# Performance work log

Hardware: AMD Instinct MI355X
Metric: run time of the kernel (lower is better)

Reference implementation:

```python
import jax, jax.numpy as jnp
import numpy as np

D_MODEL = 1024
NUM_HEADS = 16
BATCH = 2
SEQ = 2048


def setup_inputs() -> dict:
    key = jax.random.key(0)
    ks = jax.random.split(key, 5)
    scale = 1.0 / np.sqrt(D_MODEL)
    x = jax.random.normal(ks[0], (BATCH, SEQ, D_MODEL), dtype=jnp.float32)
    Wq = jax.random.normal(ks[1], (D_MODEL, D_MODEL), dtype=jnp.float32) * scale
    Wk = jax.random.normal(ks[2], (D_MODEL, D_MODEL), dtype=jnp.float32) * scale
    Wv = jax.random.normal(ks[3], (D_MODEL, D_MODEL), dtype=jnp.float32) * scale
    Wo = jax.random.normal(ks[4], (D_MODEL, D_MODEL), dtype=jnp.float32) * scale
    return {"x": x, "Wq": Wq, "Wk": Wk, "Wv": Wv, "Wo": Wo}


def reference(x, Wq, Wk, Wv, Wo):
    b, s, d_model = x.shape
    h = NUM_HEADS
    d_head = d_model // h
    # projections (Linear with weight [out,in]: y = x @ W^T)
    def split_heads(y):
        return y.reshape(b, s, h, d_head).transpose(0, 2, 1, 3)  # b h s d
    q = split_heads(x @ Wq.T)
    k = split_heads(x @ Wk.T)
    v = split_heads(x @ Wv.T)
    # full (non-flash) attention, as in the original
    att = jnp.einsum('bhsd,bhtd->bhst', q, k) / jnp.sqrt(jnp.float32(d_head)).astype(x.dtype)
    att = jax.nn.softmax(att, axis=-1)
    out = jnp.einsum('bhst,bhtd->bhsd', att, v)
    out = out.transpose(0, 2, 1, 3).reshape(b, s, d_model)
    return out @ Wo.T
```

## Files before the change

### kernel.cpp

```cpp
#include <hip/hip_runtime.h>
#include <stdint.h>

typedef __bf16 bf16_t;
typedef __bf16 bf16x4 __attribute__((ext_vector_type(4)));
typedef __bf16 bf16x8 __attribute__((ext_vector_type(8)));
typedef float  f32x4  __attribute__((ext_vector_type(4)));
typedef float  f32x16 __attribute__((ext_vector_type(16)));

#define D_MODEL 1024
#define SEQ     2048
#define BATCH   2
#define NHEAD   16
#define DHEAD   64
#define NROWS   (BATCH*SEQ)
#define LDT     72

#define QSCALE  (0.125f * 1.4426950408889634f)

__device__ __forceinline__ void async_ld16(const bf16_t* g, bf16_t* l) {
    __builtin_amdgcn_global_load_lds(
        (const __attribute__((address_space(1))) uint32_t*)(uintptr_t)g,
        (__attribute__((address_space(3))) uint32_t*)(uintptr_t)l,
        16, 0, 0);
}

__device__ __forceinline__ bf16x8 cvt8(f32x4 lo, f32x4 hi) {
    bf16x8 o;
#pragma unroll
    for (int i = 0; i < 4; ++i) { o[i] = (bf16_t)lo[i]; o[4 + i] = (bf16_t)hi[i]; }
    return o;
}

__device__ __forceinline__ void plswap(uint32_t& a, uint32_t& b) {
    asm("v_permlane32_swap_b32 %0, %1" : "+v"(a), "+v"(b));
}

__global__ void __launch_bounds__(256)
k_cvt(const float* __restrict__ w0, const float* __restrict__ w1,
      const float* __restrict__ w2, const float* __restrict__ w3,
      const float* __restrict__ x,
      bf16_t* __restrict__ o0, bf16_t* __restrict__ o1,
      bf16_t* __restrict__ o2, bf16_t* __restrict__ o3,
      bf16_t* __restrict__ ox)
{
    const int blk = blockIdx.x;
    const float* s; bf16_t* d; int bi;
    if (blk < 2048) { s = x; d = ox; bi = blk; }
    else {
        const int t = blk - 2048, sel = t >> 9; bi = t & 511;
        s = (sel == 0) ? w0 : (sel == 1) ? w1 : (sel == 2) ? w2 : w3;
        d = (sel == 0) ? o0 : (sel == 1) ? o1 : (sel == 2) ? o2 : o3;
    }
    const size_t i = ((size_t)bi * 256 + threadIdx.x) * 8;
    *(bf16x8*)(d + i) = cvt8(*(const f32x4*)(s + i), *(const f32x4*)(s + i + 4));
}

template <int OUT_MODE>
__device__ __forceinline__ void gemm128(bf16_t* __restrict__ smem,
                                        const bf16_t* __restrict__ X,
                                        const bf16_t* __restrict__ W,
                                        void* __restrict__ Yv,
                                        int m0, int n0, float oscale)
{
    bf16_t* lA = smem;
    bf16_t* lB = smem + 128 * 32;

    const int tid  = threadIdx.x;
    const int lane = tid & 63;
    const int w    = tid >> 6;
    const int l15  = lane & 15;
    const int quad = lane >> 4;

    const int c0 = tid, c1 = tid + 256;
    const int r0 = c0 >> 2, r1 = c1 >> 2;
    const int kc0 = (c0 & 3) ^ ((r0 >> 1) & 3);
    const int kc1 = (c1 & 3) ^ ((r1 >> 1) & 3);
    const bf16_t* gA0 = X + (size_t)(m0 + r0) * D_MODEL + kc0 * 8;
    const bf16_t* gA1 = X + (size_t)(m0 + r1) * D_MODEL + kc1 * 8;
    const bf16_t* gB0 = W + (size_t)(n0 + r0) * D_MODEL + kc0 * 8;
    const bf16_t* gB1 = W + (size_t)(n0 + r1) * D_MODEL + kc1 * 8;

    int am[4], bn[4];
    const int mw = (w >> 1) * 64, nw = (w & 1) * 64;
#pragma unroll
    for (int i = 0; i < 4; ++i) {
        const int ra = mw + i * 16 + l15;
        am[i] = ra * 32 + (quad ^ ((ra >> 1) & 3)) * 8;
        const int rb = nw + i * 16 + l15;
        bn[i] = rb * 32 + (quad ^ ((rb >> 1) & 3)) * 8;
    }

    f32x4 acc[4][4];
#pragma unroll
    for (int i = 0; i < 4; ++i)
#pragma unroll
        for (int j = 0; j < 4; ++j) acc[i][j] = f32x4{0.f, 0.f, 0.f, 0.f};

    for (int k0 = 0; k0 < D_MODEL; k0 += 32) {
        __syncthreads();
        async_ld16(gA0 + k0, &lA[c0 * 8]);
        async_ld16(gA1 + k0, &lA[c1 * 8]);
        async_ld16(gB0 + k0, &lB[c0 * 8]);
        async_ld16(gB1 + k0, &lB[c1 * 8]);
        __syncthreads();

        bf16x8 af[4], bfr[4];
#pragma unroll
        for (int i = 0; i < 4; ++i) af[i]  = *(const bf16x8*)&lA[am[i]];
#pragma unroll
        for (int i = 0; i < 4; ++i) bfr[i] = *(const bf16x8*)&lB[bn[i]];
#pragma unroll
        for (int mi = 0; mi < 4; ++mi)
#pragma unroll
            for (int ni = 0; ni < 4; ++ni)
                acc[mi][ni] = __builtin_amdgcn_mfma_f32_16x16x32_bf16(
                    af[mi], bfr[ni], acc[mi][ni], 0, 0, 0);
    }

    if constexpr (OUT_MODE == 1) {
        bf16_t* lT = smem;
#pragma unroll
        for (int h0 = 0; h0 < 2; ++h0) {
            __syncthreads();
            if ((w >> 1) == h0) {
#pragma unroll
                for (int mi = 0; mi < 4; ++mi)
#pragma unroll
                    for (int ni = 0; ni < 4; ++ni) {
                        bf16x4 pk;
#pragma unroll
                        for (int r = 0; r < 4; ++r)
                            pk[r] = (bf16_t)(acc[mi][ni][r] * oscale);
                        const int col = nw + ni * 16 + l15;
                        *(bf16x4*)&lT[col * LDT + mi * 16 + quad * 4] = pk;
                    }
            }
            __syncthreads();
            const int col = tid & 127;
            const int seg = tid >> 7;
            const int brow = m0 + h0 * 64;
            const int b = brow >> 11, sb = brow & 2047;
            const int cg = n0 + col;
            bf16_t* dst = (bf16_t*)Yv +
                ((size_t)((b << 4) | (cg >> 6)) * 64 + (cg & 63)) * SEQ + sb;
#pragma unroll
            for (int u = 0; u < 4; ++u)
                *(bf16x8*)(dst + seg * 32 + u * 8) =
                    *(const bf16x8*)&lT[col * LDT + seg * 32 + u * 8];
        }
    } else {
#pragma unroll
        for (int mi = 0; mi < 4; ++mi)
#pragma unroll
            for (int ni = 0; ni < 4; ++ni)
#pragma unroll
                for (int r = 0; r < 4; ++r) {
                    const int row = m0 + mw + mi * 16 + quad * 4 + r;
                    const int col = n0 + nw + ni * 16 + l15;
                    const float vv = acc[mi][ni][r] * oscale;
                    if constexpr (OUT_MODE == 0)
                        ((bf16_t*)Yv)[(size_t)row * D_MODEL + col] = (bf16_t)vv;
                    else
                        ((float*)Yv)[(size_t)row * D_MODEL + col] = vv;
                }
    }
}

__global__ void __launch_bounds__(256, 3)
k_gemm_qkv(const bf16_t* __restrict__ X,
           const bf16_t* __restrict__ Wq, const bf16_t* __restrict__ Wk,
           const bf16_t* __restrict__ Wv,
           bf16_t* __restrict__ Qb, bf16_t* __restrict__ Kb, bf16_t* __restrict__ Vt)
{
    __shared__ __align__(16) bf16_t smem[128 * LDT];
    const int sel = blockIdx.y >> 3;
    const int n0  = (blockIdx.y & 7) * 128;
    const int m0  = blockIdx.x * 128;
    if (sel == 0)      gemm128<0>(smem, X, Wq, Qb, m0, n0, QSCALE);
    else if (sel == 1) gemm128<0>(smem, X, Wk, Kb, m0, n0, 1.0f);
    else               gemm128<1>(smem, X, Wv, Vt, m0, n0, 1.0f);
}

__global__ void __launch_bounds__(256, 3)
k_gemm_out(const bf16_t* __restrict__ X, const bf16_t* __restrict__ W,
           float* __restrict__ Y)
{
    __shared__ __align__(16) bf16_t smem[128 * LDT];
    gemm128<2>(smem, X, W, Y, blockIdx.x * 128, blockIdx.y * 128, 1.0f);
}

__global__ void __launch_bounds__(256, 2)
k_attn(const bf16_t* __restrict__ Qb, const bf16_t* __restrict__ Kb,
       const bf16_t* __restrict__ Vt, bf16_t* __restrict__ Ob)
{
    __shared__ __align__(16) char arena[51200];
    bf16_t* lK = (bf16_t*)arena;
    bf16_t* lV = (bf16_t*)(arena + 16384);

    const int tid  = threadIdx.x;
    const int lane = tid & 63;
    const int w    = tid >> 6;
    const int wq   = w >> 1;
    const int wk   = w & 1;
    const int l31  = lane & 31;
    const int h    = lane >> 5;

    const int bh = blockIdx.x;
    const int b_ = bh >> 4, hh = bh & 15;
    const int q0 = blockIdx.y * 128;

    const size_t base = (size_t)b_ * SEQ * D_MODEL + (size_t)hh * DHEAD;
    const bf16_t* Qp = Qb + base;
    const bf16_t* Kp = Kb + base;
    const bf16_t* Vp = Vt + (size_t)bh * DHEAD * SEQ;

    bf16x8 qf[2][4];
#pragma unroll
    for (int qh = 0; qh < 2; ++qh) {
        const int qrow = q0 + wq * 64 + qh * 32 + l31;
#pragma unroll
        for (int c = 0; c < 4; ++c)
            qf[qh][c] = *(const bf16x8*)&Qp[(size_t)qrow * D_MODEL + c * 16 + h * 8];
    }

    const int c0 = tid, c1 = tid + 256;
    const int r0 = c0 >> 3, g0 = (c0 & 7) ^ (r0 & 7);
    const int r1 = r0 + 32;
    const bf16_t* gK0 = Kp + (size_t)r0 * D_MODEL + g0 * 8;
    const bf16_t* gK1 = Kp + (size_t)r1 * D_MODEL + g0 * 8;
    const bf16_t* gV0 = Vp + (size_t)r0 * SEQ + g0 * 8;
    const bf16_t* gV1 = Vp + (size_t)r1 * SEQ + g0 * 8;

    int koff[4], voff[2][2];
#pragma unroll
    for (int c = 0; c < 4; ++c) {
        const int row = wk * 32 + l31;
        koff[c] = row * 64 + (((2 * c + h) ^ (row & 7)) * 8);
    }
#pragma unroll
    for (int a = 0; a < 2; ++a)
#pragma unroll
        for (int ck = 0; ck < 2; ++ck) {
            const int row = a * 32 + l31;
            const int ch  = 4 * wk + 2 * ck + h;
            voff[a][ck] = row * 64 + ((ch ^ (row & 7)) * 8);
        }

    bf16x8 onef;
#pragma unroll
    for (int i = 0; i < 8; ++i) onef[i] = (bf16_t)1.0f;

    f32x16 acc_o[2][2];
    f32x16 acc_s[2];
#pragma unroll
    for (int qh = 0; qh < 2; ++qh) {
#pragma unroll
        for (int i = 0; i < 16; ++i) {
            acc_o[qh][0][i] = 0.f; acc_o[qh][1][i] = 0.f; acc_s[qh][i] = 0.f;
        }
    }

    async_ld16(gK0, &lK[c0 * 8]);
    async_ld16(gK1, &lK[c1 * 8]);
    async_ld16(gV0, &lV[c0 * 8]);
    async_ld16(gV1, &lV[c1 * 8]);
    asm volatile("s_waitcnt vmcnt(0)\n\ts_barrier" ::: "memory");

    int cur = 0;
    const int NT = SEQ / 64;
    for (int t = 0; t < NT; ++t) {
        if (t + 1 < NT) {
            const int kv0 = (t + 1) * 64;
            const int nb = (cur ^ 1) * 4096;
            async_ld16(gK0 + (size_t)kv0 * D_MODEL, &lK[nb + c0 * 8]);
            async_ld16(gK1 + (size_t)kv0 * D_MODEL, &lK[nb + c1 * 8]);
            async_ld16(gV0 + kv0, &lV[nb + c0 * 8]);
            async_ld16(gV1 + kv0, &lV[nb + c1 * 8]);
        }
        const bf16_t* lKc = lK + cur * 4096;
        const bf16_t* lVc = lV + cur * 4096;

        bf16x8 kf[4];
#pragma unroll
        for (int c = 0; c < 4; ++c) kf[c] = *(const bf16x8*)&lKc[koff[c]];

        f32x16 st[2];
#pragma unroll
        for (int qh = 0; qh < 2; ++qh)
#pragma unroll
            for (int i = 0; i < 16; ++i) st[qh][i] = 0.f;
        __builtin_amdgcn_s_setprio(1);
#pragma unroll
        for (int qh = 0; qh < 2; ++qh)
#pragma unroll
            for (int c = 0; c < 4; ++c)
                st[qh] = __builtin_amdgcn_mfma_f32_32x32x16_bf16(
                    kf[c], qf[qh][c], st[qh], 0, 0, 0);
        __builtin_amdgcn_s_setprio(0);

        bf16x4 pk[2][4];
#pragma unroll
        for (int qh = 0; qh < 2; ++qh)
#pragma unroll
            for (int g = 0; g < 4; ++g)
#pragma unroll
                for (int r = 0; r < 4; ++r)
                    pk[qh][g][r] = (bf16_t)__builtin_amdgcn_exp2f(st[qh][g * 4 + r]);

        bf16x8 pf[2][2];
#pragma unroll
        for (int qh = 0; qh < 2; ++qh)
#pragma unroll
            for (int ck = 0; ck < 2; ++ck) {
                union { bf16x4 v; uint32_t d[2]; } ua, ub;
                ua.v = pk[qh][2 * ck];
                ub.v = pk[qh][2 * ck + 1];
                uint32_t a0 = ua.d[0], b0 = ub.d[0];
                uint32_t a1 = ua.d[1], b1 = ub.d[1];
                plswap(a0, b0);
                plswap(a1, b1);
                union { bf16x8 v; uint32_t d[4]; } up;
                up.d[0] = a0; up.d[1] = a1; up.d[2] = b0; up.d[3] = b1;
                pf[qh][ck] = up.v;
            }

        __builtin_amdgcn_s_setprio(1);
#pragma unroll
        for (int qh = 0; qh < 2; ++qh)
#pragma unroll
            for (int ck = 0; ck < 2; ++ck)
                acc_s[qh] = __builtin_amdgcn_mfma_f32_32x32x16_bf16(
                    pf[qh][ck], onef, acc_s[qh], 0, 0, 0);
#pragma unroll
        for (int a = 0; a < 2; ++a)
#pragma unroll
            for (int ck = 0; ck < 2; ++ck) {
                bf16x8 vf = *(const bf16x8*)&lVc[voff[a][ck]];
#pragma unroll
                for (int qh = 0; qh < 2; ++qh)
                    acc_o[qh][a] = __builtin_amdgcn_mfma_f32_32x32x16_bf16(
                        pf[qh][ck], vf, acc_o[qh][a], 0, 0, 0);
            }
        __builtin_amdgcn_s_setprio(0);

        asm volatile("s_waitcnt vmcnt(0) lgkmcnt(0)\n\ts_barrier" ::: "memory");
        cur ^= 1;
    }

    union F16 { f32x16 v; f32x4 q[4]; };
    float* blob = (float*)arena + ((size_t)(wq * 64 + lane)) * 100;

    if (wk) {
#pragma unroll
        for (int qh = 0; qh < 2; ++qh) {
#pragma unroll
            for (int a = 0; a < 2; ++a) {
                F16 u; u.v = acc_o[qh][a];
#pragma unroll
                for (int i = 0; i < 4; ++i)
                    *(f32x4*)&blob[(qh * 8 + a * 4 + i) * 4] = u.q[i];
            }
            F16 s; s.v = acc_s[qh];
#pragma unroll
            for (int i = 0; i < 4; ++i)
                *(f32x4*)&blob[64 + (qh * 4 + i) * 4] = s.q[i];
        }
    }
    __syncthreads();
    if (!wk) {
#pragma unroll
        for (int qh = 0; qh < 2; ++qh) {
#pragma unroll
            for (int a = 0; a < 2; ++a) {
                F16 u; u.v = acc_o[qh][a];
#pragma unroll
                for (int i = 0; i < 4; ++i)
                    u.q[i] += *(const f32x4*)&blob[(qh * 8 + a * 4 + i) * 4];
                acc_o[qh][a] = u.v;
            }
            F16 s; s.v = acc_s[qh];
#pragma unroll
            for (int i = 0; i < 4; ++i)
                s.q[i] += *(const f32x4*)&blob[64 + (qh * 4 + i) * 4];
            acc_s[qh] = s.v;
        }

#pragma unroll
        for (int qh = 0; qh < 2; ++qh)
#pragma unroll
            for (int g = 0; g < 4; ++g)
#pragma unroll
                for (int r = 0; r < 4; ++r) {
                    const float inv = 1.0f / acc_s[qh][g * 4 + r];
                    const int row = b_ * SEQ + q0 + wq * 64 + qh * 32 + (r + 8 * g + 4 * h);
                    const size_t rb = (size_t)row * D_MODEL + hh * DHEAD + l31;
                    Ob[rb]      = (bf16_t)(acc_o[qh][0][g * 4 + r] * inv);
                    Ob[rb + 32] = (bf16_t)(acc_o[qh][1][g * 4 + r] * inv);
                }
    }
}

extern "C" void kernel_launch(void* const* d_in, const int* in_sizes, int n_in,
                              void* d_out, int out_size, void* d_ws, size_t ws_size,
                              hipStream_t stream)
{
    const float* x  = (const float*)d_in[0];
    const float* Wq = (const float*)d_in[1];
    const float* Wk = (const float*)d_in[2];
    const float* Wv = (const float*)d_in[3];
    const float* Wo = (const float*)d_in[4];
    float* out = (float*)d_out;

    const size_t wmat = (size_t)D_MODEL * D_MODEL;
    const size_t mat  = (size_t)NROWS * D_MODEL;
    bf16_t* Wqb = (bf16_t*)d_ws;
    bf16_t* Wkb = Wqb + wmat;
    bf16_t* Wvb = Wkb + wmat;
    bf16_t* Wob = Wvb + wmat;
    bf16_t* Xb  = Wob + wmat;
    bf16_t* Qb  = Xb + mat;
    bf16_t* Kb  = Qb + mat;
    bf16_t* Vt  = Kb + mat;
    bf16_t* Ab  = Qb;

    dim3 blk(256);
    k_cvt<<<dim3(4096), blk, 0, stream>>>(Wq, Wk, Wv, Wo, x, Wqb, Wkb, Wvb, Wob, Xb);
    k_gemm_qkv<<<dim3(32, 24), blk, 0, stream>>>(Xb, Wqb, Wkb, Wvb, Qb, Kb, Vt);
    k_attn<<<dim3(32, 16), blk, 0, stream>>>(Qb, Kb, Vt, Ab);
    k_gemm_out<<<dim3(32, 8), blk, 0, stream>>>(Ab, Wob, out);
}
```

Before: 179.1 us.

## Triple-buffer attention KV loads, remap block grids, and shrink output GEMM tile

The attention kernel moves from double to triple buffering of K/V tiles in LDS, so each iteration waits for only one outstanding stage. It also starts the score MFMA from a zero register instead of clearing it every iteration and packs exp results with v_cvt_pk_bf16_f32. The QKV, attention and output GEMM grids are remapped across blocks to change cache and XCD locality. The output GEMM uses 64-row tiles, giving twice as many blocks for better CU fill at the cost of less reuse per block. These are several independent changes and each carries its own risk, for example more LDS use per attention block.

After: 183.7 us. 1.03x slower.

```diff
diff --git a/kernel.cpp b/kernel.cpp
--- a/kernel.cpp
+++ b/kernel.cpp
@@ -35,6 +35,12 @@
     asm("v_permlane32_swap_b32 %0, %1" : "+v"(a), "+v"(b));
 }
 
+__device__ __forceinline__ uint32_t cvtpk(float lo, float hi) {
+    uint32_t r;
+    asm("v_cvt_pk_bf16_f32 %0, %1, %2" : "=v"(r) : "v"(lo), "v"(hi));
+    return r;
+}
+
 __global__ void __launch_bounds__(256)
 k_cvt(const float* __restrict__ w0, const float* __restrict__ w1,
       const float* __restrict__ w2, const float* __restrict__ w3,
@@ -55,15 +61,16 @@
     *(bf16x8*)(d + i) = cvt8(*(const f32x4*)(s + i), *(const f32x4*)(s + i + 4));
 }
 
-template <int OUT_MODE>
-__device__ __forceinline__ void gemm128(bf16_t* __restrict__ smem,
-                                        const bf16_t* __restrict__ X,
-                                        const bf16_t* __restrict__ W,
-                                        void* __restrict__ Yv,
-                                        int m0, int n0, float oscale)
-{
+template <int OUT_MODE, int MT>
+__device__ __forceinline__ void gemmT(bf16_t* __restrict__ smem,
+                                      const bf16_t* __restrict__ X,
+                                      const bf16_t* __restrict__ W,
+                                      void* __restrict__ Yv,
+                                      int m0, int n0, float oscale)
+{
+    constexpr int FM = MT / 32;
     bf16_t* lA = smem;
-    bf16_t* lB = smem + 128 * 32;
+    bf16_t* lB = smem + MT * 32;
 
     const int tid  = threadIdx.x;
     const int lane = tid & 63;
@@ -71,46 +78,56 @@
     const int l15  = lane & 15;
     const int quad = lane >> 4;
 
-    const int c0 = tid, c1 = tid + 256;
-    const int r0 = c0 >> 2, r1 = c1 >> 2;
-    const int kc0 = (c0 & 3) ^ ((r0 >> 1) & 3);
-    const int kc1 = (c1 & 3) ^ ((r1 >> 1) & 3);
-    const bf16_t* gA0 = X + (size_t)(m0 + r0) * D_MODEL + kc0 * 8;
-    const bf16_t* gA1 = X + (size_t)(m0 + r1) * D_MODEL + kc1 * 8;
-    const bf16_t* gB0 = W + (size_t)(n0 + r0) * D_MODEL + kc0 * 8;
-    const bf16_t* gB1 = W + (size_t)(n0 + r1) * D_MODEL + kc1 * 8;
-
-    int am[4], bn[4];
-    const int mw = (w >> 1) * 64, nw = (w & 1) * 64;
-#pragma unroll
-    for (int i = 0; i < 4; ++i) {
+    const int cB0 = tid, cB1 = tid + 256;
+    const int rB0 = cB0 >> 2, rB1 = cB1 >> 2;
+    const int kB0 = (cB0 & 3) ^ ((rB0 >> 1) & 3);
+    const int kB1 = (cB1 & 3) ^ ((rB1 >> 1) & 3);
+    const bf16_t* gB0 = W + (size_t)(n0 + rB0) * D_MODEL + kB0 * 8;
+    const bf16_t* gB1 = W + (size_t)(n0 + rB1) * D_MODEL + kB1 * 8;
+
+    const int cA0 = tid;
+    const int rA0 = cA0 >> 2;
+    const int kA0 = (cA0 & 3) ^ ((rA0 >> 1) & 3);
+    const bf16_t* gA0 = X + (size_t)(m0 + rA0) * D_MODEL + kA0 * 8;
+    const int cA1 = tid + 256;
+    const int rA1 = cA1 >> 2;
+    const int kA1 = (cA1 & 3) ^ ((rA1 >> 1) & 3);
+    const bf16_t* gA1 = X + (size_t)(m0 + rA1) * D_MODEL + kA1 * 8;
+
+    int am[FM], bn[4];
+    const int mw = (w >> 1) * (MT / 2), nw = (w & 1) * 64;
+#pragma unroll
+    for (int i = 0; i < FM; ++i) {
         const int ra = mw + i * 16 + l15;
         am[i] = ra * 32 + (quad ^ ((ra >> 1) & 3)) * 8;
+    }
+#pragma unroll
+    for (int i = 0; i < 4; ++i) {
         const int rb = nw + i * 16 + l15;
         bn[i] = rb * 32 + (quad ^ ((rb >> 1) & 3)) * 8;
     }
 
-    f32x4 acc[4][4];
-#pragma unroll
-    for (int i = 0; i < 4; ++i)
+    f32x4 acc[FM][4];
+#pragma unroll
+    for (int i = 0; i < FM; ++i)
 #pragma unroll
         for (int j = 0; j < 4; ++j) acc[i][j] = f32x4{0.f, 0.f, 0.f, 0.f};
 
     for (int k0 = 0; k0 < D_MODEL; k0 += 32) {
         __syncthreads();
-        async_ld16(gA0 + k0, &lA[c0 * 8]);
-        async_ld16(gA1 + k0, &lA[c1 * 8]);
-        async_ld16(gB0 + k0, &lB[c0 * 8]);
-        async_ld16(gB1 + k0, &lB[c1 * 8]);
+        async_ld16(gA0 + k0, &lA[cA0 * 8]);
+        if constexpr (MT == 128) async_ld16(gA1 + k0, &lA[cA1 * 8]);
+        async_ld16(gB0 + k0, &lB[cB0 * 8]);
+        async_ld16(gB1 + k0, &lB[cB1 * 8]);
         __syncthreads();
 
-        bf16x8 af[4], bfr[4];
-#pragma unroll
-        for (int i = 0; i < 4; ++i) af[i]  = *(const bf16x8*)&lA[am[i]];
+        bf16x8 af[FM], bfr[4];
+#pragma unroll
+        for (int i = 0; i < FM; ++i) af[i] = *(const bf16x8*)&lA[am[i]];
 #pragma unroll
         for (int i = 0; i < 4; ++i) bfr[i] = *(const bf16x8*)&lB[bn[i]];
 #pragma unroll
-        for (int mi = 0; mi < 4; ++mi)
+        for (int mi = 0; mi < FM; ++mi)
 #pragma unroll
             for (int ni = 0; ni < 4; ++ni)
                 acc[mi][ni] = __builtin_amdgcn_mfma_f32_16x16x32_bf16(
@@ -124,7 +141,7 @@
             __syncthreads();
             if ((w >> 1) == h0) {
 #pragma unroll
-                for (int mi = 0; mi < 4; ++mi)
+                for (int mi = 0; mi < FM; ++mi)
 #pragma unroll
                     for (int ni = 0; ni < 4; ++ni) {
                         bf16x4 pk;
@@ -150,7 +167,7 @@
         }
     } else {
 #pragma unroll
-        for (int mi = 0; mi < 4; ++mi)
+        for (int mi = 0; mi < FM; ++mi)
 #pragma unroll
             for (int ni = 0; ni < 4; ++ni)
 #pragma unroll
@@ -173,20 +190,27 @@
            bf16_t* __restrict__ Qb, bf16_t* __restrict__ Kb, bf16_t* __restrict__ Vt)
 {
     __shared__ __align__(16) bf16_t smem[128 * LDT];
-    const int sel = blockIdx.y >> 3;
-    const int n0  = (blockIdx.y & 7) * 128;
-    const int m0  = blockIdx.x * 128;
-    if (sel == 0)      gemm128<0>(smem, X, Wq, Qb, m0, n0, QSCALE);
-    else if (sel == 1) gemm128<0>(smem, X, Wk, Kb, m0, n0, 1.0f);
-    else               gemm128<1>(smem, X, Wv, Vt, m0, n0, 1.0f);
-}
-
-__global__ void __launch_bounds__(256, 3)
+    const int id = blockIdx.x + 32 * blockIdx.y;
+    const int s  = (id & 7) * 96 + (id >> 3);
+    const int m0 = (s & 31) * 128;
+    const int yp = s >> 5;
+    const int sel = yp >> 3;
+    const int n0  = (yp & 7) * 128;
+    if (sel == 0)      gemmT<0,128>(smem, X, Wq, Qb, m0, n0, QSCALE);
+    else if (sel == 1) gemmT<0,128>(smem, X, Wk, Kb, m0, n0, 1.0f);
+    else               gemmT<1,128>(smem, X, Wv, Vt, m0, n0, 1.0f);
+}
+
+__global__ void __launch_bounds__(256, 2)
 k_gemm_out(const bf16_t* __restrict__ X, const bf16_t* __restrict__ W,
            float* __restrict__ Y)
 {
-    __shared__ __align__(16) bf16_t smem[128 * LDT];
-    gemm128<2>(smem, X, W, Y, blockIdx.x * 128, blockIdx.y * 128, 1.0f);
+    __shared__ __align__(16) bf16_t smem[64 * 32 + 128 * 32];
+    const int id = blockIdx.x + 64 * blockIdx.y;
+    const int s  = (id & 7) * 64 + (id >> 3);
+    const int m0 = (s & 63) * 64;
+    const int n0 = (s >> 6) * 128;
+    gemmT<2,64>(smem, X, W, Y, m0, n0, 1.0f);
 }
 
 __global__ void __launch_bounds__(256, 2)
@@ -195,7 +219,7 @@
 {
     __shared__ __align__(16) char arena[51200];
     bf16_t* lK = (bf16_t*)arena;
-    bf16_t* lV = (bf16_t*)(arena + 16384);
+    bf16_t* lV = (bf16_t*)(arena + 24576);
 
     const int tid  = threadIdx.x;
     const int lane = tid & 63;
@@ -205,9 +229,10 @@
     const int l31  = lane & 31;
     const int h    = lane >> 5;
 
-    const int bh = blockIdx.x;
+    const int i_  = blockIdx.x + 32 * blockIdx.y;
+    const int bh  = 4 * (i_ & 7) + ((i_ >> 3) & 3);
+    const int q0  = (i_ >> 5) * 128;
     const int b_ = bh >> 4, hh = bh & 15;
-    const int q0 = blockIdx.y * 128;
 
     const size_t base = (size_t)b_ * SEQ * D_MODEL + (size_t)hh * DHEAD;
     const bf16_t* Qp = Qb + base;
@@ -250,6 +275,10 @@
 #pragma unroll
     for (int i = 0; i < 8; ++i) onef[i] = (bf16_t)1.0f;
 
+    f32x16 fz;
+#pragma unroll
+    for (int i = 0; i < 16; ++i) fz[i] = 0.f;
+
     f32x16 acc_o[2][2];
     f32x16 acc_s[2];
 #pragma unroll
@@ -260,63 +289,62 @@
         }
     }
 
-    async_ld16(gK0, &lK[c0 * 8]);
-    async_ld16(gK1, &lK[c1 * 8]);
-    async_ld16(gV0, &lV[c0 * 8]);
-    async_ld16(gV1, &lV[c1 * 8]);
-    asm volatile("s_waitcnt vmcnt(0)\n\ts_barrier" ::: "memory");
-
-    int cur = 0;
+    auto STAGE = [&](int tile, int buf) {
+        const size_t kv0 = (size_t)tile * 64;
+        bf16_t* dK = lK + buf * 4096;
+        bf16_t* dV = lV + buf * 4096;
+        async_ld16(gK0 + kv0 * D_MODEL, &dK[c0 * 8]);
+        async_ld16(gK1 + kv0 * D_MODEL, &dK[c1 * 8]);
+        async_ld16(gV0 + kv0, &dV[c0 * 8]);
+        async_ld16(gV1 + kv0, &dV[c1 * 8]);
+    };
+
+    STAGE(0, 0);
+    STAGE(1, 1);
+    asm volatile("s_waitcnt vmcnt(4)\n\ts_barrier" ::: "memory");
+
+    int cb = 0;
     const int NT = SEQ / 64;
     for (int t = 0; t < NT; ++t) {
-        if (t + 1 < NT) {
-            const int kv0 = (t + 1) * 64;
-            const int nb = (cur ^ 1) * 4096;
-            async_ld16(gK0 + (size_t)kv0 * D_MODEL, &lK[nb + c0 * 8]);
-            async_ld16(gK1 + (size_t)kv0 * D_MODEL, &lK[nb + c1 * 8]);
-            async_ld16(gV0 + kv0, &lV[nb + c0 * 8]);
-            async_ld16(gV1 + kv0, &lV[nb + c1 * 8]);
-        }
-        const bf16_t* lKc = lK + cur * 4096;
-        const bf16_t* lVc = lV + cur * 4096;
+        if (t + 2 < NT) STAGE(t + 2, cb == 0 ? 2 : cb - 1);
+        const bf16_t* lKc = lK + cb * 4096;
+        const bf16_t* lVc = lV + cb * 4096;
 
         bf16x8 kf[4];
 #pragma unroll
         for (int c = 0; c < 4; ++c) kf[c] = *(const bf16x8*)&lKc[koff[c]];
 
         f32x16 st[2];
-#pragma unroll
-        for (int qh = 0; qh < 2; ++qh)
-#pragma unroll
-            for (int i = 0; i < 16; ++i) st[qh][i] = 0.f;
         __builtin_amdgcn_s_setprio(1);
 #pragma unroll
-        for (int qh = 0; qh < 2; ++qh)
-#pragma unroll
-            for (int c = 0; c < 4; ++c)
+        for (int qh = 0; qh < 2; ++qh) {
+            st[qh] = __builtin_amdgcn_mfma_f32_32x32x16_bf16(
+                kf[0], qf[qh][0], fz, 0, 0, 0);
+#pragma unroll
+            for (int c = 1; c < 4; ++c)
                 st[qh] = __builtin_amdgcn_mfma_f32_32x32x16_bf16(
                     kf[c], qf[qh][c], st[qh], 0, 0, 0);
+        }
         __builtin_amdgcn_s_setprio(0);
 
-        bf16x4 pk[2][4];
+        uint32_t pd[2][4][2];
 #pragma unroll
         for (int qh = 0; qh < 2; ++qh)
 #pragma unroll
-            for (int g = 0; g < 4; ++g)
-#pragma unroll
-                for (int r = 0; r < 4; ++r)
-                    pk[qh][g][r] = (bf16_t)__builtin_amdgcn_exp2f(st[qh][g * 4 + r]);
+            for (int g = 0; g < 4; ++g) {
+                pd[qh][g][0] = cvtpk(__builtin_amdgcn_exp2f(st[qh][g * 4 + 0]),
+                                     __builtin_amdgcn_exp2f(st[qh][g * 4 + 1]));
+                pd[qh][g][1] = cvtpk(__builtin_amdgcn_exp2f(st[qh][g * 4 + 2]),
+                                     __builtin_amdgcn_exp2f(st[qh][g * 4 + 3]));
+            }
 
         bf16x8 pf[2][2];
 #pragma unroll
         for (int qh = 0; qh < 2; ++qh)
 #pragma unroll
             for (int ck = 0; ck < 2; ++ck) {
-                union { bf16x4 v; uint32_t d[2]; } ua, ub;
-                ua.v = pk[qh][2 * ck];
-                ub.v = pk[qh][2 * ck + 1];
-                uint32_t a0 = ua.d[0], b0 = ub.d[0];
-                uint32_t a1 = ua.d[1], b1 = ub.d[1];
+                uint32_t a0 = pd[qh][2 * ck][0],     b0 = pd[qh][2 * ck + 1][0];
+                uint32_t a1 = pd[qh][2 * ck][1],     b1 = pd[qh][2 * ck + 1][1];
                 plswap(a0, b0);
                 plswap(a1, b1);
                 union { bf16x8 v; uint32_t d[4]; } up;
@@ -343,8 +371,11 @@
             }
         __builtin_amdgcn_s_setprio(0);
 
-        asm volatile("s_waitcnt vmcnt(0) lgkmcnt(0)\n\ts_barrier" ::: "memory");
-        cur ^= 1;
+        if (t + 2 < NT)
+            asm volatile("s_waitcnt vmcnt(4) lgkmcnt(0)\n\ts_barrier" ::: "memory");
+        else
+            asm volatile("s_waitcnt vmcnt(0) lgkmcnt(0)\n\ts_barrier" ::: "memory");
+        cb = (cb == 2) ? 0 : cb + 1;
     }
 
     union F16 { f32x16 v; f32x4 q[4]; };
@@ -427,5 +458,5 @@
     k_cvt<<<dim3(4096), blk, 0, stream>>>(Wq, Wk, Wv, Wo, x, Wqb, Wkb, Wvb, Wob, Xb);
     k_gemm_qkv<<<dim3(32, 24), blk, 0, stream>>>(Xb, Wqb, Wkb, Wvb, Qb, Kb, Vt);
     k_attn<<<dim3(32, 16), blk, 0, stream>>>(Qb, Kb, Vt, Ab);
-    k_gemm_out<<<dim3(32, 8), blk, 0, stream>>>(Ab, Wob, out);
-}
+    k_gemm_out<<<dim3(64, 8), blk, 0, stream>>>(Ab, Wob, out);
+}
```
